# Kernel tuning notes

Measured on AMD Instinct MI355X. Metric: run time of the kernel, lower is better.

Reference implementation:

```python
import jax, jax.numpy as jnp
import numpy as np

B, L, V, H, D = 32, 2048, 512, 1024, 512
NNZ_PER_B = 512  # valid source positions per batch row


def setup_inputs() -> dict:
    key = jax.random.key(0)
    k1, k2, k3, k4, k5, k6 = jax.random.split(key, 6)
    # sparse pattern: NNZ_PER_B positions per batch (guarantees no empty row)
    idx0 = jnp.repeat(jnp.arange(B, dtype=jnp.int64), NNZ_PER_B)
    idx1 = jax.random.randint(k1, (B * NNZ_PER_B,), 0, L).astype(jnp.int64)
    sparse_indices = jnp.stack([idx0, idx1])  # [2, nnz]
    mask = jnp.zeros((B, L), bool).at[idx0, idx1].set(True)
    dhs = jax.random.normal(k2, (B, H), jnp.float32)
    # dense input is zero outside the sparse pattern (matches to_sparse dropping zeros)
    bdi = jax.random.normal(k3, (B, L, V), jnp.float32) * mask[..., None]
    att = jax.random.normal(k4, (B, L, D), jnp.float32)
    W1 = jax.random.normal(k5, (V, H), jnp.float32) / np.sqrt(H)   # Linear(H, V).weight
    W2 = jax.random.normal(k6, (V, 1), jnp.float32) / np.sqrt(V)   # Linear(V, 1).weight^T
    return {
        "Decoder_Hidden_State": dhs,
        "Batch_decoder_input_hh": bdi,
        "Batch_Decoder_Input_Attender": att,
        "sparse_indices": sparse_indices,
        "sparse_val": 0,
        "W1": W1,
        "W2": W2,
    }


def reference(Decoder_Hidden_State, Batch_decoder_input_hh, Batch_Decoder_Input_Attender,
              sparse_indices, sparse_val, W1, W2):
    b, l, v = Batch_decoder_input_hh.shape
    # decoder_hidden_state_mlp: [B,H] @ [H,V] -> [B,V]
    dec = Decoder_Hidden_State @ W1.T
    # scatter the per-batch vector into the sparse (b,l) positions
    mask = jnp.zeros((b, l), bool).at[sparse_indices[0], sparse_indices[1]].set(True)
    hh_sparse = jnp.where(mask[..., None], dec[:, None, :], 0.0)  # [B,L,V]
    in_hh = Batch_decoder_input_hh if sparse_val == 1 else Batch_decoder_input_hh + hh_sparse
    sum_val = hh_sparse + in_hh
    # decoder_mapper_mlp -> scores [B,L,1]; sparse softmax over L = masked softmax
    scores = sum_val @ W2
    s = jnp.where(mask[..., None], scores, -jnp.inf)
    alpha = jax.nn.softmax(s, axis=1)
    alpha = jnp.where(mask[..., None], alpha, 0.0)  # [B,L,1], zero off-pattern
    # sparse weighted sum over L -> [B,D]
    c = jnp.sum(Batch_Decoder_Input_Attender * alpha, axis=1)
    return c, alpha
```

## Files before the change

### kernel.cpp

```cpp
#include <hip/hip_runtime.h>
#include <math.h>

#define B 32
#define L 2048
#define V 512
#define D 512
#define S_CTX 32
#define CAP 512


__global__ __launch_bounds__(256) void k_init(float* __restrict__ scores,
        float* __restrict__ c, const int* __restrict__ idx32, int nnz,
        int* __restrict__ flag) {
    int i = blockIdx.x * 256 + threadIdx.x;
    if (i < B * L) scores[i] = -INFINITY;
    if (i < B * D) c[i] = 0.f;
    if (blockIdx.x == 0 && threadIdx.x < 64) {
        int step = nnz / 128; if (step < 1) step = 1;
        int w = nnz + 1 + 2 * threadIdx.x * step;
        unsigned long long nz = __ballot(idx32[w] != 0);
        if (threadIdx.x == 0) *flag = (nz == 0ull) ? 1 : 0;
    }
}

__global__ __launch_bounds__(256) void k_scores(const float* __restrict__ bdi,
        const float* __restrict__ W2, const void* __restrict__ idx, int nnz,
        const int* __restrict__ flag, float* __restrict__ scores) {
    int wave = threadIdx.x >> 6, lane = threadIdx.x & 63;
    int e = blockIdx.x * 4 + wave;
    if (e >= nnz) return;
    int b, l;
    if (*flag) {
        const long long* q = (const long long*)idx;
        b = (int)q[e];
        l = (int)q[nnz + e];
    } else {
        const int* q = (const int*)idx;
        b = q[e];
        l = q[nnz + e];
    }
    const float4* row = (const float4*)(bdi + ((size_t)b * L + l) * V);
    const float4* w   = (const float4*)W2;
    float4 r0 = row[lane],      w0 = w[lane];
    float4 r1 = row[lane + 64], w1 = w[lane + 64];
    float acc = r0.x * w0.x + r0.y * w0.y + r0.z * w0.z + r0.w * w0.w
              + r1.x * w1.x + r1.y * w1.y + r1.z * w1.z + r1.w * w1.w;
    for (int off = 32; off; off >>= 1) acc += __shfl_down(acc, off, 64);
    if (lane == 0) scores[b * L + l] = acc;
}

__global__ __launch_bounds__(256) void k_softmax(const float* __restrict__ scores,
        float* __restrict__ alpha, int* __restrict__ clist,
        float* __restrict__ cval, int* __restrict__ wcnt) {
    int b = blockIdx.x, tid = threadIdx.x;
    __shared__ float e_s[L];
    __shared__ float red[256];
    __shared__ int cnt;
    if (tid == 0) cnt = 0;
    const float4* sv = (const float4*)(scores + b * L);
    float4 v0 = sv[tid], v1 = sv[tid + 256];
    ((float4*)e_s)[tid] = v0;
    ((float4*)e_s)[tid + 256] = v1;
    float m = fmaxf(fmaxf(fmaxf(v0.x, v0.y), fmaxf(v0.z, v0.w)),
                    fmaxf(fmaxf(v1.x, v1.y), fmaxf(v1.z, v1.w)));
    red[tid] = m;
    __syncthreads();
    for (int off = 128; off; off >>= 1) {
        if (tid < off) red[tid] = fmaxf(red[tid], red[tid + off]);
        __syncthreads();
    }
    m = red[0];
    __syncthreads();
    float sum = 0.f;
    for (int l = tid; l < L; l += 256) {
        float e = __expf(e_s[l] - m);
        e_s[l] = e;
        sum += e;
    }
    red[tid] = sum;
    __syncthreads();
    for (int off = 128; off; off >>= 1) {
        if (tid < off) red[tid] += red[tid + off];
        __syncthreads();
    }
    float inv = 1.f / red[0];
    __syncthreads();
    float4* av = (float4*)(alpha + b * L);
    #pragma unroll
    for (int seg = 0; seg < 2; ++seg) {
        int q = tid + seg * 256;
        float4 e4 = ((const float4*)e_s)[q];
        float4 a4 = {e4.x * inv, e4.y * inv, e4.z * inv, e4.w * inv};
        av[q] = a4;
        float av_[4] = {a4.x, a4.y, a4.z, a4.w};
        #pragma unroll
        for (int k = 0; k < 4; ++k) {
            if (av_[k] > 0.f) {
                int p = atomicAdd(&cnt, 1);
                clist[b * CAP + p] = q * 4 + k;
                cval[b * CAP + p]  = av_[k];
            }
        }
    }
    __syncthreads();
    if (tid == 0) wcnt[b] = cnt;
}

__global__ __launch_bounds__(256) void k_context(const float* __restrict__ att,
        const int* __restrict__ clist, const float* __restrict__ cval,
        const int* __restrict__ wcnt, float* __restrict__ c) {
    int b = blockIdx.x / S_CTX, s = blockIdx.x % S_CTX;
    int n = wcnt[b];
    int half = threadIdx.x >> 7;
    int dq   = threadIdx.x & 127;
    float4 acc = {0.f, 0.f, 0.f, 0.f};
    for (int j0 = s * 2; j0 < n; j0 += S_CTX * 2) {
        int j = j0 + half;
        if (j < n) {
            int   l = clist[b * CAP + j];
            float a = cval[b * CAP + j];
            float4 v = *(const float4*)(att + ((size_t)b * L + l) * D + dq * 4);
            acc.x += a * v.x;
            acc.y += a * v.y;
            acc.z += a * v.z;
            acc.w += a * v.w;
        }
    }
    float* cb = c + b * D + dq * 4;
    atomicAdd(cb + 0, acc.x);
    atomicAdd(cb + 1, acc.y);
    atomicAdd(cb + 2, acc.z);
    atomicAdd(cb + 3, acc.w);
}

extern "C" void kernel_launch(void* const* d_in, const int* in_sizes, int n_in,
                              void* d_out, int out_size, void* d_ws, size_t ws_size,
                              hipStream_t stream) {
    const float* bdi  = (const float*)d_in[1];
    const float* att  = (const float*)d_in[2];
    const void*  sidx = d_in[3];
    const float* W2   = (const float*)d_in[6];

    float* out   = (float*)d_out;
    float* c     = out;
    float* alpha = out + B * D;
    int nnz = in_sizes[3] / 2;

    char* ws = (char*)d_ws;
    int*   flag   = (int*)ws;
    int*   wcnt   = (int*)(ws + 256);
    float* scores = (float*)(ws + 1024);
    int*   clist  = (int*)(ws + 1024 + B * L * 4);
    float* cval   = (float*)(ws + 1024 + B * L * 4 + B * CAP * 4);

    k_init<<<(B * L + 255) / 256, 256, 0, stream>>>(scores, c, (const int*)sidx, nnz, flag);
    k_scores<<<(nnz + 3) / 4, 256, 0, stream>>>(bdi, W2, sidx, nnz, flag, scores);
    k_softmax<<<B, 256, 0, stream>>>(scores, alpha, clist, cval, wcnt);
    k_context<<<B * S_CTX, 256, 0, stream>>>(att, clist, cval, wcnt, c);
}
```

Measured before the change: 260.7 us.

## Fuse sparse softmax into context kernel using compact per-batch score lists

The scores kernel now dedups (b,l) positions with an atomicCAS claim array and appends each score to a compact per-batch list, replacing the dense score buffer. The separate softmax kernel is removed. Each context block recomputes the softmax over its batch's compact list, at most 512 entries, and writes its share of alpha directly. This drops a launch and the dense L-length scan per batch, at the cost of redundant softmax work in every context block and extra atomics.

```diff
diff --git a/kernel.cpp b/kernel.cpp
--- a/kernel.cpp
+++ b/kernel.cpp
@@ -9,12 +9,15 @@
 #define CAP 512
 
 
-__global__ __launch_bounds__(256) void k_init(float* __restrict__ scores,
-        float* __restrict__ c, const int* __restrict__ idx32, int nnz,
+__global__ __launch_bounds__(256) void k_init(float* __restrict__ alpha,
+        float* __restrict__ c, unsigned int* __restrict__ claim,
+        int* __restrict__ cnt, const int* __restrict__ idx32, int nnz,
         int* __restrict__ flag) {
     int i = blockIdx.x * 256 + threadIdx.x;
-    if (i < B * L) scores[i] = -INFINITY;
+    alpha[i] = 0.f;
+    claim[i] = 0u;
     if (i < B * D) c[i] = 0.f;
+    if (i < B) cnt[i] = 0;
     if (blockIdx.x == 0 && threadIdx.x < 64) {
         int step = nnz / 128; if (step < 1) step = 1;
         int w = nnz + 1 + 2 * threadIdx.x * step;
@@ -25,7 +28,8 @@
 
 __global__ __launch_bounds__(256) void k_scores(const float* __restrict__ bdi,
         const float* __restrict__ W2, const void* __restrict__ idx, int nnz,
-        const int* __restrict__ flag, float* __restrict__ scores) {
+        const int* __restrict__ flag, unsigned int* __restrict__ claim,
+        int* __restrict__ cnt, int* __restrict__ slist, float* __restrict__ sval) {
     int wave = threadIdx.x >> 6, lane = threadIdx.x & 63;
     int e = blockIdx.x * 4 + wave;
     if (e >= nnz) return;
@@ -39,87 +43,67 @@
         b = q[e];
         l = q[nnz + e];
     }
-    const float4* row = (const float4*)(bdi + ((size_t)b * L + l) * V);
+    int bl = b * L + l;
+    int win = 0;
+    if (lane == 0) win = (atomicCAS(&claim[bl], 0u, 1u) == 0u) ? 1 : 0;
+    win = __shfl(win, 0, 64);
+    if (!win) return;
+    const float4* row = (const float4*)(bdi + (size_t)bl * V);
     const float4* w   = (const float4*)W2;
     float4 r0 = row[lane],      w0 = w[lane];
     float4 r1 = row[lane + 64], w1 = w[lane + 64];
     float acc = r0.x * w0.x + r0.y * w0.y + r0.z * w0.z + r0.w * w0.w
               + r1.x * w1.x + r1.y * w1.y + r1.z * w1.z + r1.w * w1.w;
     for (int off = 32; off; off >>= 1) acc += __shfl_down(acc, off, 64);
-    if (lane == 0) scores[b * L + l] = acc;
+    if (lane == 0) {
+        int p = atomicAdd(&cnt[b], 1);
+        slist[b * CAP + p] = l;
+        sval[b * CAP + p]  = acc;
+    }
 }
 
-__global__ __launch_bounds__(256) void k_softmax(const float* __restrict__ scores,
-        float* __restrict__ alpha, int* __restrict__ clist,
-        float* __restrict__ cval, int* __restrict__ wcnt) {
-    int b = blockIdx.x, tid = threadIdx.x;
-    __shared__ float e_s[L];
+__global__ __launch_bounds__(256) void k_ctx(const float* __restrict__ att,
+        const int* __restrict__ cnt, const int* __restrict__ slist,
+        const float* __restrict__ sval, float* __restrict__ alpha,
+        float* __restrict__ c) {
+    int b = blockIdx.x / S_CTX, s = blockIdx.x % S_CTX;
+    int tid = threadIdx.x;
+    __shared__ int   l_s[CAP];
+    __shared__ float e_s[CAP];
     __shared__ float red[256];
-    __shared__ int cnt;
-    if (tid == 0) cnt = 0;
-    const float4* sv = (const float4*)(scores + b * L);
-    float4 v0 = sv[tid], v1 = sv[tid + 256];
-    ((float4*)e_s)[tid] = v0;
-    ((float4*)e_s)[tid + 256] = v1;
-    float m = fmaxf(fmaxf(fmaxf(v0.x, v0.y), fmaxf(v0.z, v0.w)),
-                    fmaxf(fmaxf(v1.x, v1.y), fmaxf(v1.z, v1.w)));
-    red[tid] = m;
+    int n = cnt[b];
+    int j0 = tid, j1 = tid + 256;
+    float s0 = -INFINITY, s1 = -INFINITY;
+    if (j0 < n) { l_s[j0] = slist[b * CAP + j0]; s0 = sval[b * CAP + j0]; }
+    if (j1 < n) { l_s[j1] = slist[b * CAP + j1]; s1 = sval[b * CAP + j1]; }
+    red[tid] = fmaxf(s0, s1);
     __syncthreads();
     for (int off = 128; off; off >>= 1) {
         if (tid < off) red[tid] = fmaxf(red[tid], red[tid + off]);
         __syncthreads();
     }
-    m = red[0];
+    float m = red[0];
     __syncthreads();
-    float sum = 0.f;
-    for (int l = tid; l < L; l += 256) {
-        float e = __expf(e_s[l] - m);
-        e_s[l] = e;
-        sum += e;
-    }
-    red[tid] = sum;
+    float e0 = (j0 < n) ? __expf(s0 - m) : 0.f;
+    float e1 = (j1 < n) ? __expf(s1 - m) : 0.f;
+    if (j0 < n) e_s[j0] = e0;
+    if (j1 < n) e_s[j1] = e1;
+    red[tid] = e0 + e1;
     __syncthreads();
     for (int off = 128; off; off >>= 1) {
         if (tid < off) red[tid] += red[tid + off];
         __syncthreads();
     }
     float inv = 1.f / red[0];
-    __syncthreads();
-    float4* av = (float4*)(alpha + b * L);
-    #pragma unroll
-    for (int seg = 0; seg < 2; ++seg) {
-        int q = tid + seg * 256;
-        float4 e4 = ((const float4*)e_s)[q];
-        float4 a4 = {e4.x * inv, e4.y * inv, e4.z * inv, e4.w * inv};
-        av[q] = a4;
-        float av_[4] = {a4.x, a4.y, a4.z, a4.w};
-        #pragma unroll
-        for (int k = 0; k < 4; ++k) {
-            if (av_[k] > 0.f) {
-                int p = atomicAdd(&cnt, 1);
-                clist[b * CAP + p] = q * 4 + k;
-                cval[b * CAP + p]  = av_[k];
-            }
-        }
-    }
-    __syncthreads();
-    if (tid == 0) wcnt[b] = cnt;
-}
-
-__global__ __launch_bounds__(256) void k_context(const float* __restrict__ att,
-        const int* __restrict__ clist, const float* __restrict__ cval,
-        const int* __restrict__ wcnt, float* __restrict__ c) {
-    int b = blockIdx.x / S_CTX, s = blockIdx.x % S_CTX;
-    int n = wcnt[b];
-    int half = threadIdx.x >> 7;
-    int dq   = threadIdx.x & 127;
+    if (j0 < n && (j0 & (S_CTX - 1)) == s) alpha[b * L + l_s[j0]] = e0 * inv;
+    if (j1 < n && (j1 & (S_CTX - 1)) == s) alpha[b * L + l_s[j1]] = e1 * inv;
+    int half = tid >> 7, dq = tid & 127;
     float4 acc = {0.f, 0.f, 0.f, 0.f};
-    for (int j0 = s * 2; j0 < n; j0 += S_CTX * 2) {
-        int j = j0 + half;
+    for (int jj = s * 2; jj < n; jj += S_CTX * 2) {
+        int j = jj + half;
         if (j < n) {
-            int   l = clist[b * CAP + j];
-            float a = cval[b * CAP + j];
-            float4 v = *(const float4*)(att + ((size_t)b * L + l) * D + dq * 4);
+            float a = e_s[j] * inv;
+            float4 v = *(const float4*)(att + ((size_t)b * L + l_s[j]) * D + dq * 4);
             acc.x += a * v.x;
             acc.y += a * v.y;
             acc.z += a * v.z;
@@ -147,14 +131,13 @@
     int nnz = in_sizes[3] / 2;
 
     char* ws = (char*)d_ws;
-    int*   flag   = (int*)ws;
-    int*   wcnt   = (int*)(ws + 256);
-    float* scores = (float*)(ws + 1024);
-    int*   clist  = (int*)(ws + 1024 + B * L * 4);
-    float* cval   = (float*)(ws + 1024 + B * L * 4 + B * CAP * 4);
+    int*          flag  = (int*)ws;
+    int*          cnt   = (int*)(ws + 64);
+    unsigned int* claim = (unsigned int*)(ws + 1024);
+    int*          slist = (int*)(ws + 1024 + B * L * 4);
+    float*        sval  = (float*)(ws + 1024 + B * L * 4 + B * CAP * 4);
 
-    k_init<<<(B * L + 255) / 256, 256, 0, stream>>>(scores, c, (const int*)sidx, nnz, flag);
-    k_scores<<<(nnz + 3) / 4, 256, 0, stream>>>(bdi, W2, sidx, nnz, flag, scores);
-    k_softmax<<<B, 256, 0, stream>>>(scores, alpha, clist, cval, wcnt);
-    k_context<<<B * S_CTX, 256, 0, stream>>>(att, clist, cval, wcnt, c);
+    k_init<<<B * L / 256, 256, 0, stream>>>(alpha, c, claim, cnt, (const int*)sidx, nnz, flag);
+    k_scores<<<(nnz + 3) / 4, 256, 0, stream>>>(bdi, W2, sidx, nnz, flag, claim, cnt, slist, sval);
+    k_ctx<<<B * S_CTX, 256, 0, stream>>>(att, cnt, slist, sval, alpha, c);
 }
```

After: 405.1 us. 1.55x slower.

## Fuse masked softmax into context kernel with per-block redundant row reductions

Applied to the files above, without the earlier changes.

Merges the softmax and context kernels into one launch. Each of the 32 blocks per batch row recomputes the row max and sum, then compacts the nonzero positions of its own 64-element slice into shared memory and accumulates the weighted attender rows. This drops one kernel launch and the global compaction lists, at the cost of 32x redundant reduction work per row.

```diff
diff --git a/kernel.cpp b/kernel.cpp
--- a/kernel.cpp
+++ b/kernel.cpp
@@ -6,14 +6,14 @@
 #define V 512
 #define D 512
 #define S_CTX 32
-#define CAP 512
+#define SH   (L / S_CTX)
 
 
 __global__ __launch_bounds__(256) void k_init(float* __restrict__ scores,
         float* __restrict__ c, const int* __restrict__ idx32, int nnz,
         int* __restrict__ flag) {
     int i = blockIdx.x * 256 + threadIdx.x;
-    if (i < B * L) scores[i] = -INFINITY;
+    scores[i] = -INFINITY;
     if (i < B * D) c[i] = 0.f;
     if (blockIdx.x == 0 && threadIdx.x < 64) {
         int step = nnz / 128; if (step < 1) step = 1;
@@ -49,18 +49,19 @@
     if (lane == 0) scores[b * L + l] = acc;
 }
 
-__global__ __launch_bounds__(256) void k_softmax(const float* __restrict__ scores,
-        float* __restrict__ alpha, int* __restrict__ clist,
-        float* __restrict__ cval, int* __restrict__ wcnt) {
-    int b = blockIdx.x, tid = threadIdx.x;
+__global__ __launch_bounds__(256) void k_ctx(const float* __restrict__ att,
+        const float* __restrict__ scores, float* __restrict__ alpha,
+        float* __restrict__ c) {
+    int b = blockIdx.x >> 5, s = blockIdx.x & (S_CTX - 1);
+    int tid = threadIdx.x;
     __shared__ float e_s[L];
     __shared__ float red[256];
+    __shared__ int   l_c[SH];
+    __shared__ float a_c[SH];
     __shared__ int cnt;
     if (tid == 0) cnt = 0;
-    const float4* sv = (const float4*)(scores + b * L);
-    float4 v0 = sv[tid], v1 = sv[tid + 256];
-    ((float4*)e_s)[tid] = v0;
-    ((float4*)e_s)[tid + 256] = v1;
+    const float4* srow = (const float4*)(scores + b * L);
+    float4 v0 = srow[tid], v1 = srow[tid + 256];
     float m = fmaxf(fmaxf(fmaxf(v0.x, v0.y), fmaxf(v0.z, v0.w)),
                     fmaxf(fmaxf(v1.x, v1.y), fmaxf(v1.z, v1.w)));
     red[tid] = m;
@@ -71,60 +72,45 @@
     }
     m = red[0];
     __syncthreads();
-    float sum = 0.f;
-    for (int l = tid; l < L; l += 256) {
-        float e = __expf(e_s[l] - m);
-        e_s[l] = e;
-        sum += e;
-    }
-    red[tid] = sum;
+    float4 e0, e1;
+    e0.x = __expf(v0.x - m); e0.y = __expf(v0.y - m);
+    e0.z = __expf(v0.z - m); e0.w = __expf(v0.w - m);
+    e1.x = __expf(v1.x - m); e1.y = __expf(v1.y - m);
+    e1.z = __expf(v1.z - m); e1.w = __expf(v1.w - m);
+    ((float4*)e_s)[tid]       = e0;
+    ((float4*)e_s)[tid + 256] = e1;
+    red[tid] = e0.x + e0.y + e0.z + e0.w + e1.x + e1.y + e1.z + e1.w;
     __syncthreads();
     for (int off = 128; off; off >>= 1) {
         if (tid < off) red[tid] += red[tid + off];
         __syncthreads();
     }
     float inv = 1.f / red[0];
-    __syncthreads();
-    float4* av = (float4*)(alpha + b * L);
-    #pragma unroll
-    for (int seg = 0; seg < 2; ++seg) {
-        int q = tid + seg * 256;
-        float4 e4 = ((const float4*)e_s)[q];
-        float4 a4 = {e4.x * inv, e4.y * inv, e4.z * inv, e4.w * inv};
-        av[q] = a4;
-        float av_[4] = {a4.x, a4.y, a4.z, a4.w};
-        #pragma unroll
-        for (int k = 0; k < 4; ++k) {
-            if (av_[k] > 0.f) {
-                int p = atomicAdd(&cnt, 1);
-                clist[b * CAP + p] = q * 4 + k;
-                cval[b * CAP + p]  = av_[k];
-            }
+    if (tid < SH) {
+        int l = s * SH + tid;
+        float e = e_s[l];
+        if (e > 0.f) {
+            int p = atomicAdd(&cnt, 1);
+            l_c[p] = l;
+            a_c[p] = e * inv;
         }
     }
+    if (tid < SH / 4) {
+        float4 ev = ((const float4*)e_s)[s * (SH / 4) + tid];
+        float4 av = {ev.x * inv, ev.y * inv, ev.z * inv, ev.w * inv};
+        ((float4*)(alpha + b * L))[s * (SH / 4) + tid] = av;
+    }
     __syncthreads();
-    if (tid == 0) wcnt[b] = cnt;
-}
-
-__global__ __launch_bounds__(256) void k_context(const float* __restrict__ att,
-        const int* __restrict__ clist, const float* __restrict__ cval,
-        const int* __restrict__ wcnt, float* __restrict__ c) {
-    int b = blockIdx.x / S_CTX, s = blockIdx.x % S_CTX;
-    int n = wcnt[b];
-    int half = threadIdx.x >> 7;
-    int dq   = threadIdx.x & 127;
+    int n = cnt;
+    int half = tid >> 7, dq = tid & 127;
     float4 acc = {0.f, 0.f, 0.f, 0.f};
-    for (int j0 = s * 2; j0 < n; j0 += S_CTX * 2) {
-        int j = j0 + half;
-        if (j < n) {
-            int   l = clist[b * CAP + j];
-            float a = cval[b * CAP + j];
-            float4 v = *(const float4*)(att + ((size_t)b * L + l) * D + dq * 4);
-            acc.x += a * v.x;
-            acc.y += a * v.y;
-            acc.z += a * v.z;
-            acc.w += a * v.w;
-        }
+    for (int j = half; j < n; j += 2) {
+        float a = a_c[j];
+        float4 v = *(const float4*)(att + ((size_t)b * L + l_c[j]) * D + dq * 4);
+        acc.x += a * v.x;
+        acc.y += a * v.y;
+        acc.z += a * v.z;
+        acc.w += a * v.w;
     }
     float* cb = c + b * D + dq * 4;
     atomicAdd(cb + 0, acc.x);
@@ -148,13 +134,9 @@
 
     char* ws = (char*)d_ws;
     int*   flag   = (int*)ws;
-    int*   wcnt   = (int*)(ws + 256);
     float* scores = (float*)(ws + 1024);
-    int*   clist  = (int*)(ws + 1024 + B * L * 4);
-    float* cval   = (float*)(ws + 1024 + B * L * 4 + B * CAP * 4);
 
-    k_init<<<(B * L + 255) / 256, 256, 0, stream>>>(scores, c, (const int*)sidx, nnz, flag);
+    k_init<<<B * L / 256, 256, 0, stream>>>(scores, c, (const int*)sidx, nnz, flag);
     k_scores<<<(nnz + 3) / 4, 256, 0, stream>>>(bdi, W2, sidx, nnz, flag, scores);
-    k_softmax<<<B, 256, 0, stream>>>(scores, alpha, clist, cval, wcnt);
-    k_context<<<B * S_CTX, 256, 0, stream>>>(att, clist, cval, wcnt, c);
+    k_ctx<<<B * S_CTX, 256, 0, stream>>>(att, scores, alpha, c);
 }
```

Result: faster. 254.8 us (-2.3%).
